# Performance work log

Hardware: AMD Instinct MI355X
Metric: run time of the kernel (lower is better)

Reference implementation:

```python
import jax, jax.numpy as jnp
import numpy as np

C = 256; G = 16; GC = C // G; K = 3; P = K * K
N = 4; H = 64; W = 64
PAD = 1; OFFSET_SCALE = 1.0; LN_EPS = 1e-5


def setup_inputs() -> dict:
    key = jax.random.key(0)
    ks = jax.random.split(key, 8)
    s = 0.02
    return {
        "x": jax.random.normal(ks[0], (N, C, H, W), jnp.float32),
        "dw_w": jax.random.normal(ks[1], (C, 1, K, K), jnp.float32) * s,
        "dw_b": jnp.zeros((C,), jnp.float32),
        "ln_g": jnp.ones((C,), jnp.float32),
        "ln_b": jnp.zeros((C,), jnp.float32),
        "off_w": jax.random.normal(ks[2], (C, G * P * 2), jnp.float32) * s,
        "off_b": jnp.zeros((G * P * 2,), jnp.float32),
        "mask_w": jax.random.normal(ks[3], (C, G * P), jnp.float32) * s,
        "mask_b": jnp.zeros((G * P,), jnp.float32),
        "inp_w": jax.random.normal(ks[4], (C, C), jnp.float32) * s,
        "inp_b": jnp.zeros((C,), jnp.float32),
        "out_w": jax.random.normal(ks[5], (C, C), jnp.float32) * s,
        "out_b": jnp.zeros((C,), jnp.float32),
    }


def _dcnv3_nchw(x, dw_w, dw_b, ln_g, ln_b, off_w, off_b, mask_w, mask_b,
                inp_w, inp_b, out_w, out_b):
    # NCHW -> NHWC (wrapper permute)
    xn = jnp.transpose(x, (0, 2, 3, 1))                      # (N,H,W,C)
    x_proj = xn @ inp_w + inp_b                              # input_proj

    # offset/mask branch: depthwise conv (NCHW) -> LayerNorm (channels-last) -> GELU
    x1 = jax.lax.conv_general_dilated(
        x, dw_w, window_strides=(1, 1), padding=((PAD, PAD), (PAD, PAD)),
        dimension_numbers=("NCHW", "OIHW", "NCHW"), feature_group_count=C)
    x1 = jnp.transpose(x1, (0, 2, 3, 1)) + dw_b
    mu = x1.mean(-1, keepdims=True)
    var = ((x1 - mu) ** 2).mean(-1, keepdims=True)
    x1 = (x1 - mu) * jax.lax.rsqrt(var + LN_EPS) * ln_g + ln_b
    x1 = jax.nn.gelu(x1, approximate=False)

    offset = (x1 @ off_w + off_b).reshape(N, H, W, G, P, 2)  # (x,y) pairs
    mask = jax.nn.softmax((x1 @ mask_w + mask_b).reshape(N, H, W, G, P), axis=-1)

    # pad sampled feature map with zeros (F.pad before sampling)
    xp = jnp.pad(x_proj, ((0, 0), (PAD, PAD), (PAD, PAD), (0, 0)))
    Hin, Win = H + 2 * PAD, W + 2 * PAD
    xg = xp.reshape(N, Hin, Win, G, GC)

    # reference points, normalized by padded size
    ref_y = (jnp.arange(H, dtype=jnp.float32) + PAD + 0.5) / Hin
    ref_x = (jnp.arange(W, dtype=jnp.float32) + PAD + 0.5) / Win
    ref = jnp.stack([jnp.broadcast_to(ref_x[None, :], (H, W)),
                     jnp.broadcast_to(ref_y[:, None], (H, W))], -1)  # (H,W,2)

    # dilation grid: x varies in the outer loop (torch meshgrid 'ij')
    d = jnp.arange(K, dtype=jnp.float32) - (K - 1) // 2     # [-1,0,1]
    gx = jnp.repeat(d, K) / Win
    gy = jnp.tile(d, K) / Hin
    grid = jnp.stack([gx, gy], -1)                           # (P,2)

    norm = jnp.array([Win, Hin], jnp.float32)
    loc = (ref[None, :, :, None, None, :] + grid * OFFSET_SCALE
           + offset * OFFSET_SCALE / norm)                   # (N,H,W,G,P,2)

    # grid_sample bilinear, align_corners=False, zero padding
    px = loc[..., 0] * Win - 0.5
    py = loc[..., 1] * Hin - 0.5
    x0 = jnp.floor(px); y0 = jnp.floor(py)
    wx = px - x0; wy = py - y0
    x0i = x0.astype(jnp.int32); y0i = y0.astype(jnp.int32)

    n_idx = jnp.arange(N)[:, None, None, None, None]
    g_idx = jnp.arange(G)[None, None, None, :, None]

    def corner(iy, ix, w):
        valid = (iy >= 0) & (iy < Hin) & (ix >= 0) & (ix < Win)
        v = xg[n_idx, jnp.clip(iy, 0, Hin - 1), jnp.clip(ix, 0, Win - 1), g_idx]
        wgt = jnp.where(valid, w, 0.0) * mask                # fold mask into weights
        return jnp.einsum("nhwgp,nhwgpc->nhwgc", wgt, v)

    out = (corner(y0i, x0i, (1 - wy) * (1 - wx))
           + corner(y0i, x0i + 1, (1 - wy) * wx)
           + corner(y0i + 1, x0i, wy * (1 - wx))
           + corner(y0i + 1, x0i + 1, wy * wx))               # (N,H,W,G,GC)

    out = out.reshape(N, H, W, C) @ out_w + out_b            # output_proj
    return jnp.transpose(out, (0, 3, 1, 2))                  # NHWC -> NCHW


def reference(x, dw_w, dw_b, ln_g, ln_b, off_w, off_b, mask_w, mask_b,
              inp_w, inp_b, out_w, out_b):
    return _dcnv3_nchw(x, dw_w, dw_b, ln_g, ln_b, off_w, off_b,
                       mask_w, mask_b, inp_w, inp_b, out_w, out_b)
```

## Files before the change

kernel.cpp:

```cpp
#include <hip/hip_runtime.h>
#include <hip/hip_bf16.h>
#include <math.h>


using bf16x8 = __attribute__((ext_vector_type(8))) short;
using f32x4  = __attribute__((ext_vector_type(4))) float;

#define GLOBAL_AS __attribute__((address_space(1)))
#define LDS_AS    __attribute__((address_space(3)))

static __device__ inline void g2lds16(const void* g, void* l) {
  __builtin_amdgcn_global_load_lds((const GLOBAL_AS int*)g, (LDS_AS int*)l, 16, 0, 0);
}
static __device__ inline unsigned short f2bf(float v) {
  __hip_bfloat16 b = __float2bfloat16(v);
  return *reinterpret_cast<unsigned short*>(&b);
}
static __device__ inline float us2f(unsigned short u) {
  union { unsigned u; float f; } c; c.u = ((unsigned)u) << 16; return c.f;
}

__global__ __launch_bounds__(256) void prep_k(
    const float* __restrict__ inp_w, const float* __restrict__ off_w,
    const float* __restrict__ off_b, const float* __restrict__ mask_w,
    const float* __restrict__ mask_b, const float* __restrict__ out_w,
    __hip_bfloat16* __restrict__ BtI, __hip_bfloat16* __restrict__ BtOM,
    __hip_bfloat16* __restrict__ BtO, float* __restrict__ bOM)
{
  int b = blockIdx.x, t = threadIdx.x;
  if (b < 256) {
    int n = b;
    BtI[n * 256 + t] = __float2bfloat16(inp_w[t * 256 + n]);
  } else if (b < 768) {
    int n = b - 256;
    float v = 0.f;
    if (n < 288) v = off_w[t * 288 + n];
    else if (n < 432) v = mask_w[t * 144 + (n - 288)];
    BtOM[n * 256 + t] = __float2bfloat16(v);
    if (b == 256) {
      for (int idx = t; idx < 512; idx += 256) {
        float bv = (idx < 288) ? off_b[idx] : ((idx < 432) ? mask_b[idx - 288] : 0.f);
        bOM[idx] = bv;
      }
    }
  } else {
    int n = b - 768;
    BtO[n * 256 + t] = __float2bfloat16(out_w[t * 256 + n]);
  }
}

__global__ __launch_bounds__(256) void xt_k(const float* __restrict__ x,
                                            __hip_bfloat16* __restrict__ xT) {
  __shared__ float tile[32][65];
  const int hw0 = blockIdx.x * 64, c0 = blockIdx.y * 32, n4 = blockIdx.z;
  const int t = threadIdx.x;
  #pragma unroll
  for (int r = 0; r < 8; ++r) {
    int idx = t + r * 256;
    int cl = idx >> 6, wl = idx & 63;
    tile[cl][wl] = x[(size_t)n4 * 1048576 + (size_t)(c0 + cl) * 4096 + hw0 + wl];
  }
  __syncthreads();
  #pragma unroll
  for (int r = 0; r < 2; ++r) {
    int idx = t + r * 256;
    int pixl = idx >> 3, cq = idx & 7;
    unsigned short b0 = f2bf(tile[cq * 4 + 0][pixl]);
    unsigned short b1 = f2bf(tile[cq * 4 + 1][pixl]);
    unsigned short b2 = f2bf(tile[cq * 4 + 2][pixl]);
    unsigned short b3 = f2bf(tile[cq * 4 + 3][pixl]);
    uint2 u;
    u.x = (unsigned)b0 | ((unsigned)b1 << 16);
    u.y = (unsigned)b2 | ((unsigned)b3 << 16);
    *(uint2*)&xT[((size_t)n4 * 4096 + hw0 + pixl) * 256 + c0 + cq * 4] = u;
  }
}

template<int CMODE>
__global__ __launch_bounds__(256) void gemm_mfma(
    const __hip_bfloat16* __restrict__ A, const __hip_bfloat16* __restrict__ Bt,
    const float* __restrict__ bias, void* __restrict__ Cv, int ldc, int nstore)
{
  __shared__ __align__(16) char smem[16512];
  short* As = (short*)smem;
  short* Bs = (short*)(smem + 8192);
  float* tb = (float*)smem;
  const int t = threadIdx.x;
  const int wave = t >> 6, lane = t & 63;
  const int quad = lane >> 4, lr = lane & 15;
  const int wm = wave >> 1, wn = wave & 1;
  const size_t m0 = (size_t)blockIdx.y * 128;
  const int n0 = blockIdx.x * 128;

  f32x4 acc[4][4];
  #pragma unroll
  for (int i = 0; i < 4; ++i)
    #pragma unroll
    for (int j = 0; j < 4; ++j)
      acc[i][j] = (f32x4){0.f, 0.f, 0.f, 0.f};

  const int srow = wave * 32;
  for (int kt = 0; kt < 256; kt += 32) {
    #pragma unroll
    for (int j = 0; j < 2; ++j) {
      int chunk = j * 64 + lane;
      int row = srow + (chunk >> 2), kq = chunk & 3;
      const __hip_bfloat16* gA = A + (m0 + row) * 256 + kt + kq * 8;
      const __hip_bfloat16* gB = Bt + (size_t)(n0 + row) * 256 + kt + kq * 8;
      g2lds16(gA, (char*)As + wave * 2048 + j * 1024);
      g2lds16(gB, (char*)Bs + wave * 2048 + j * 1024);
    }
    __syncthreads();
    bf16x8 bfv[4];
    #pragma unroll
    for (int ni = 0; ni < 4; ++ni)
      bfv[ni] = *(const bf16x8*)&Bs[(wn * 64 + ni * 16 + lr) * 32 + quad * 8];
    #pragma unroll
    for (int mi = 0; mi < 4; ++mi) {
      bf16x8 af = *(const bf16x8*)&As[(wm * 64 + mi * 16 + lr) * 32 + quad * 8];
      #pragma unroll
      for (int ni = 0; ni < 4; ++ni)
        acc[mi][ni] = __builtin_amdgcn_mfma_f32_16x16x32_bf16(af, bfv[ni], acc[mi][ni], 0, 0, 0);
    }
    __syncthreads();
  }

  if (CMODE == 2) {
    #pragma unroll
    for (int mi = 0; mi < 4; ++mi) {
      #pragma unroll
      for (int ni = 0; ni < 4; ++ni) {
        int col = n0 + wn * 64 + ni * 16 + lr;
        if (col < nstore) {
          float bv = bias[col];
          #pragma unroll
          for (int reg = 0; reg < 4; ++reg) {
            size_t m = m0 + wm * 64 + mi * 16 + quad * 4 + reg;
            ((__hip_bfloat16*)Cv)[m * ldc + col] =
                __float2bfloat16(acc[mi][ni][reg] + bv);
          }
        }
      }
    }
  } else {
    const int n4 = (int)(m0 >> 12), hw0 = (int)(m0 & 4095);
    for (int qc = 0; qc < 4; ++qc) {
      __syncthreads();
      if (wn == (qc >> 1)) {
        #pragma unroll
        for (int nis = 0; nis < 2; ++nis) {
          int ni = 2 * (qc & 1) + nis;
          int col = n0 + wn * 64 + ni * 16 + lr;
          float bv = bias[col];
          int cl = nis * 16 + lr;
          #pragma unroll
          for (int mi = 0; mi < 4; ++mi)
            #pragma unroll
            for (int reg = 0; reg < 4; ++reg) {
              int ml = wm * 64 + mi * 16 + quad * 4 + reg;
              tb[cl * 129 + ml] = acc[mi][ni][reg] + bv;
            }
        }
      }
      __syncthreads();
      #pragma unroll
      for (int r = 0; r < 4; ++r) {
        int f4i = t + r * 256;
        int row = f4i >> 5, mc = (f4i & 31) * 4;
        int co = n0 + qc * 32 + row;
        float4 v;
        v.x = tb[row * 129 + mc + 0];
        v.y = tb[row * 129 + mc + 1];
        v.z = tb[row * 129 + mc + 2];
        v.w = tb[row * 129 + mc + 3];
        *(float4*)&((float*)Cv)[(size_t)(n4 * 256 + co) * 4096 + hw0 + mc] = v;
      }
    }
  }
}

__global__ __launch_bounds__(256) void dwconv_k(
    const float* __restrict__ x, const float* __restrict__ dw_w,
    const float* __restrict__ dw_b, __hip_bfloat16* __restrict__ y)
{
  __shared__ float pl[4096];
  const int bc = blockIdx.x;
  const int n4 = bc >> 8, c = bc & 255;
  const int t = threadIdx.x;
  const float* xc = x + (size_t)n4 * 1048576 + (size_t)c * 4096;
  #pragma unroll
  for (int r = 0; r < 4; ++r) {
    int idx4 = t + r * 256;
    *(float4*)&pl[idx4 * 4] = *(const float4*)&xc[idx4 * 4];
  }
  float wv[9];
  #pragma unroll
  for (int i = 0; i < 9; ++i) wv[i] = dw_w[c * 9 + i];
  const float bb = dw_b[c];
  __syncthreads();
  __hip_bfloat16* yc = y + (size_t)(n4 * 256 + c) * 4096;
  #pragma unroll 4
  for (int r = 0; r < 16; ++r) {
    int px = t + r * 256;
    int h = px >> 6, w = px & 63;
    float s = bb;
    #pragma unroll
    for (int dh = -1; dh <= 1; ++dh) {
      int hh = h + dh;
      if ((unsigned)hh >= 64u) continue;
      #pragma unroll
      for (int dw = -1; dw <= 1; ++dw) {
        int ww = w + dw;
        if ((unsigned)ww >= 64u) continue;
        s = fmaf(pl[hh * 64 + ww], wv[(dh + 1) * 3 + (dw + 1)], s);
      }
    }
    yc[px] = __float2bfloat16(s);
  }
}

__global__ __launch_bounds__(1024) void ln_k(
    const __hip_bfloat16* __restrict__ y, const float* __restrict__ ln_g,
    const float* __restrict__ ln_b, __hip_bfloat16* __restrict__ x1)
{
  __shared__ unsigned short ys[256 * 66];
  __shared__ float gs[256], bs2[256];
  __shared__ float ps[16][64], pq[16][64], mu_s[64], rs_s[64];
  const int blk = blockIdx.x;
  const int n4 = blk >> 6, h = blk & 63;
  const int t = threadIdx.x;

  if (t < 256) { gs[t] = ln_g[t]; bs2[t] = ln_b[t]; }

  const __hip_bfloat16* yb = y + (size_t)n4 * 1048576 + h * 64;
  #pragma unroll
  for (int r = 0; r < 2; ++r) {
    int idx = t + r * 1024;
    int c = idx >> 3, w8 = idx & 7;
    uint4 u = *(const uint4*)(yb + (size_t)c * 4096 + w8 * 8);
    unsigned* d = (unsigned*)&ys[c * 66 + w8 * 8];
    d[0] = u.x; d[1] = u.y; d[2] = u.z; d[3] = u.w;
  }
  __syncthreads();

  const int w = t & 63, q = t >> 6;
  {
    float s1 = 0.f, s2 = 0.f;
    #pragma unroll
    for (int i = 0; i < 16; ++i) {
      float v = us2f(ys[(q * 16 + i) * 66 + w]);
      s1 += v; s2 = fmaf(v, v, s2);
    }
    ps[q][w] = s1; pq[q][w] = s2;
  }
  __syncthreads();
  if (t < 64) {
    float a = 0.f, b = 0.f;
    #pragma unroll
    for (int j = 0; j < 16; ++j) { a += ps[j][t]; b += pq[j][t]; }
    float mu = a * (1.f / 256.f);
    mu_s[t] = mu;
    rs_s[t] = rsqrtf(b * (1.f / 256.f) - mu * mu + 1e-5f);
  }
  __syncthreads();

  const float mu = mu_s[w], rs = rs_s[w];
  #pragma unroll
  for (int i = 0; i < 16; ++i) {
    int c = q * 16 + i;
    float v = us2f(ys[c * 66 + w]);
    float yv = fmaf((v - mu) * rs, gs[c], bs2[c]);
    float ge = 0.5f * yv * (1.f + erff(yv * 0.70710678f));
    ys[c * 66 + w] = f2bf(ge);
  }
  __syncthreads();

  const size_t row0 = ((size_t)n4 * 4096 + (size_t)h * 64) * 256;
  #pragma unroll
  for (int r = 0; r < 2; ++r) {
    int idx = t + r * 1024;
    int pix = idx >> 5, co8 = idx & 31;
    unsigned short v0 = ys[(co8 * 8 + 0) * 66 + pix];
    unsigned short v1 = ys[(co8 * 8 + 1) * 66 + pix];
    unsigned short v2 = ys[(co8 * 8 + 2) * 66 + pix];
    unsigned short v3 = ys[(co8 * 8 + 3) * 66 + pix];
    unsigned short v4 = ys[(co8 * 8 + 4) * 66 + pix];
    unsigned short v5 = ys[(co8 * 8 + 5) * 66 + pix];
    unsigned short v6 = ys[(co8 * 8 + 6) * 66 + pix];
    unsigned short v7 = ys[(co8 * 8 + 7) * 66 + pix];
    uint4 u;
    u.x = (unsigned)v0 | ((unsigned)v1 << 16);
    u.y = (unsigned)v2 | ((unsigned)v3 << 16);
    u.z = (unsigned)v4 | ((unsigned)v5 << 16);
    u.w = (unsigned)v6 | ((unsigned)v7 << 16);
    *(uint4*)&x1[row0 + (size_t)pix * 256 + co8 * 8] = u;
  }
}

__global__ __launch_bounds__(256) void sample_k(
    const __hip_bfloat16* __restrict__ xpu, const __hip_bfloat16* __restrict__ om,
    __hip_bfloat16* __restrict__ samp)
{
  __shared__ unsigned short oms[16 * 448];
  const int bid = blockIdx.x;
  const int region = bid & 7;
  const int q = bid >> 3;
  const int pix0 = region * 2048 + q * 16;
  const int t = threadIdx.x;

  {
    const uint4* gsrc = (const uint4*)(om + (size_t)pix0 * 448);
    uint4* ldst = (uint4*)oms;
    #pragma unroll
    for (int r = 0; r < 4; ++r) {
      int i = t + r * 256;
      if (i < 896) ldst[i] = gsrc[i];
    }
  }
  __syncthreads();

  const int g = t & 15;
  const int pl = t >> 4;
  const int pix = pix0 + pl;
  const int n4 = pix >> 12;
  const int hw = pix & 4095;
  const int h = hw >> 6, w = hw & 63;

  float mk[9];
  {
    const unsigned short* mp = &oms[pl * 448 + 288 + g * 9];
    float mx = -1e30f;
    #pragma unroll
    for (int p = 0; p < 9; ++p) { mk[p] = us2f(mp[p]); mx = fmaxf(mx, mk[p]); }
    float se = 0.f;
    #pragma unroll
    for (int p = 0; p < 9; ++p) { mk[p] = __expf(mk[p] - mx); se += mk[p]; }
    float inv = 1.f / se;
    #pragma unroll
    for (int p = 0; p < 9; ++p) mk[p] *= inv;
  }

  const unsigned short* op = &oms[pl * 448 + g * 18];
  const __hip_bfloat16* xpg = xpu + (g << 4);
  float ax[16];
  #pragma unroll
  for (int i = 0; i < 16; ++i) ax[i] = 0.f;

  auto corner = [&](int iy, int ix, float wt) {
    if ((unsigned)(iy - 1) >= 64u || (unsigned)(ix - 1) >= 64u) return;
    const __hip_bfloat16* src =
        xpg + ((size_t)((n4 << 12) + (iy - 1) * 64 + (ix - 1)) << 8);
    uint4 u0 = *(const uint4*)src;
    uint4 u1 = *(const uint4*)(src + 8);
    const unsigned uu[8] = {u0.x, u0.y, u0.z, u0.w, u1.x, u1.y, u1.z, u1.w};
    #pragma unroll
    for (int i = 0; i < 8; ++i) {
      float lo = us2f((unsigned short)(uu[i] & 0xffff));
      float hi = us2f((unsigned short)(uu[i] >> 16));
      ax[2 * i + 0] = fmaf(wt, lo, ax[2 * i + 0]);
      ax[2 * i + 1] = fmaf(wt, hi, ax[2 * i + 1]);
    }
  };

  #pragma unroll
  for (int p = 0; p < 9; ++p) {
    float ox = us2f(op[2 * p]), oy = us2f(op[2 * p + 1]);
    float px = (float)(w + p / 3) + ox;
    float py = (float)(h + p % 3) + oy;
    float xf = floorf(px), yf = floorf(py);
    float wx = px - xf, wy = py - yf;
    int ix = (int)xf, iy = (int)yf;
    float m = mk[p];
    corner(iy,     ix,     (1.f - wy) * (1.f - wx) * m);
    corner(iy,     ix + 1, (1.f - wy) * wx * m);
    corner(iy + 1, ix,     wy * (1.f - wx) * m);
    corner(iy + 1, ix + 1, wy * wx * m);
  }

  unsigned short ub[16];
  #pragma unroll
  for (int i = 0; i < 16; ++i) ub[i] = f2bf(ax[i]);
  uint4* d4 = (uint4*)(samp + (size_t)pix * 256 + (g << 4));
  uint4 u0, u1;
  u0.x = (unsigned)ub[0] | ((unsigned)ub[1] << 16);
  u0.y = (unsigned)ub[2] | ((unsigned)ub[3] << 16);
  u0.z = (unsigned)ub[4] | ((unsigned)ub[5] << 16);
  u0.w = (unsigned)ub[6] | ((unsigned)ub[7] << 16);
  u1.x = (unsigned)ub[8] | ((unsigned)ub[9] << 16);
  u1.y = (unsigned)ub[10] | ((unsigned)ub[11] << 16);
  u1.z = (unsigned)ub[12] | ((unsigned)ub[13] << 16);
  u1.w = (unsigned)ub[14] | ((unsigned)ub[15] << 16);
  d4[0] = u0; d4[1] = u1;
}

extern "C" void kernel_launch(void* const* d_in, const int* in_sizes, int n_in,
                              void* d_out, int out_size, void* d_ws, size_t ws_size,
                              hipStream_t stream) {
  const float* x      = (const float*)d_in[0];
  const float* dw_w   = (const float*)d_in[1];
  const float* dw_b   = (const float*)d_in[2];
  const float* ln_g   = (const float*)d_in[3];
  const float* ln_b   = (const float*)d_in[4];
  const float* off_w  = (const float*)d_in[5];
  const float* off_b  = (const float*)d_in[6];
  const float* mask_w = (const float*)d_in[7];
  const float* mask_b = (const float*)d_in[8];
  const float* inp_w  = (const float*)d_in[9];
  const float* inp_b  = (const float*)d_in[10];
  const float* out_w  = (const float*)d_in[11];
  const float* out_b  = (const float*)d_in[12];
  float* out = (float*)d_out;

  char* w0 = (char*)d_ws;
  __hip_bfloat16* xpu  = (__hip_bfloat16*)(w0);
  __hip_bfloat16* y    = (__hip_bfloat16*)(w0 + 8388608);
  __hip_bfloat16* x1   = (__hip_bfloat16*)(w0 + 16777216);
  __hip_bfloat16* xT   = (__hip_bfloat16*)(w0 + 25165824);
  __hip_bfloat16* samp = xT;
  __hip_bfloat16* om   = (__hip_bfloat16*)(w0 + 33554432);
  __hip_bfloat16* BtI  = (__hip_bfloat16*)(w0 + 48234496);
  __hip_bfloat16* BtOM = (__hip_bfloat16*)(w0 + 48365568);
  __hip_bfloat16* BtO  = (__hip_bfloat16*)(w0 + 48627712);
  float*          bOM  = (float*)(w0 + 48758784);
  if (ws_size < 48760832) return;

  prep_k<<<1024, 256, 0, stream>>>(inp_w, off_w, off_b, mask_w, mask_b, out_w,
                                   BtI, BtOM, BtO, bOM);
  xt_k<<<dim3(64, 8, 4), 256, 0, stream>>>(x, xT);
  gemm_mfma<2><<<dim3(2, 128), 256, 0, stream>>>(xT, BtI, inp_b, xpu, 256, 256);
  dwconv_k<<<1024, 256, 0, stream>>>(x, dw_w, dw_b, y);
  ln_k<<<256, 1024, 0, stream>>>(y, ln_g, ln_b, x1);
  gemm_mfma<2><<<dim3(4, 128), 256, 0, stream>>>(x1, BtOM, bOM, om, 448, 432);
  sample_k<<<1024, 256, 0, stream>>>(xpu, om, samp);
  gemm_mfma<3><<<dim3(2, 128), 256, 0, stream>>>(samp, BtO, out_b, out, 0, 256);
}
```

Before: 173.0 us.

## Shrink GEMM tiles to 64x64 and merge input/offset-mask projections into one launch

Replaces the 128x128-tile MFMA GEMM template with 64x64-tile kernels, giving four to eight times as many blocks. The input projection and the offset/mask projection now share one launch that picks its operands from blockIdx.x, which removes a launch and lets the two GEMMs run at the same time on the 256 CUs. The output projection uses the smaller tile with a resized LDS transpose epilogue. The price is less data reuse per block and more global loads of the A and B tiles per unit of MFMA work.

Result: faster. 168.7 us (-2.5%).

```diff
diff --git a/kernel.cpp b/kernel.cpp
--- a/kernel.cpp
+++ b/kernel.cpp
@@ -76,105 +76,127 @@
   }
 }
 
-template<int CMODE>
-__global__ __launch_bounds__(256) void gemm_mfma(
-    const __hip_bfloat16* __restrict__ A, const __hip_bfloat16* __restrict__ Bt,
-    const float* __restrict__ bias, void* __restrict__ Cv, int ldc, int nstore)
-{
-  __shared__ __align__(16) char smem[16512];
+struct G64 {
+  f32x4 acc[2][2];
+  int wave, lane, quad, lr, wm, wn;
+};
+
+static __device__ inline void g64_loop(
+    G64& g, const __hip_bfloat16* __restrict__ A,
+    const __hip_bfloat16* __restrict__ Bt, size_t m0, int n0,
+    short* As, short* Bs, int t)
+{
+  #pragma unroll
+  for (int i = 0; i < 2; ++i)
+    #pragma unroll
+    for (int j = 0; j < 2; ++j)
+      g.acc[i][j] = (f32x4){0.f, 0.f, 0.f, 0.f};
+  const int row = t >> 2, kq = t & 3;
+  for (int kt = 0; kt < 256; kt += 32) {
+    g2lds16(A + (m0 + row) * 256 + kt + kq * 8, (char*)As + t * 16);
+    g2lds16(Bt + (size_t)(n0 + row) * 256 + kt + kq * 8, (char*)Bs + t * 16);
+    __syncthreads();
+    bf16x8 bfv[2];
+    #pragma unroll
+    for (int ni = 0; ni < 2; ++ni)
+      bfv[ni] = *(const bf16x8*)&Bs[(g.wn * 32 + ni * 16 + g.lr) * 32 + g.quad * 8];
+    #pragma unroll
+    for (int mi = 0; mi < 2; ++mi) {
+      bf16x8 af = *(const bf16x8*)&As[(g.wm * 32 + mi * 16 + g.lr) * 32 + g.quad * 8];
+      #pragma unroll
+      for (int ni = 0; ni < 2; ++ni)
+        g.acc[mi][ni] = __builtin_amdgcn_mfma_f32_16x16x32_bf16(af, bfv[ni], g.acc[mi][ni], 0, 0, 0);
+    }
+    __syncthreads();
+  }
+}
+
+__global__ __launch_bounds__(256) void gemm_iom(
+    const __hip_bfloat16* __restrict__ xT, const __hip_bfloat16* __restrict__ x1,
+    const __hip_bfloat16* __restrict__ BtI, const __hip_bfloat16* __restrict__ BtOM,
+    const float* __restrict__ inp_b, const float* __restrict__ bOM,
+    __hip_bfloat16* __restrict__ xpu, __hip_bfloat16* __restrict__ om)
+{
+  __shared__ __align__(16) char smem[8192];
   short* As = (short*)smem;
-  short* Bs = (short*)(smem + 8192);
-  float* tb = (float*)smem;
-  const int t = threadIdx.x;
-  const int wave = t >> 6, lane = t & 63;
-  const int quad = lane >> 4, lr = lane & 15;
-  const int wm = wave >> 1, wn = wave & 1;
-  const size_t m0 = (size_t)blockIdx.y * 128;
-  const int n0 = blockIdx.x * 128;
-
-  f32x4 acc[4][4];
-  #pragma unroll
-  for (int i = 0; i < 4; ++i)
-    #pragma unroll
-    for (int j = 0; j < 4; ++j)
-      acc[i][j] = (f32x4){0.f, 0.f, 0.f, 0.f};
-
-  const int srow = wave * 32;
-  for (int kt = 0; kt < 256; kt += 32) {
-    #pragma unroll
-    for (int j = 0; j < 2; ++j) {
-      int chunk = j * 64 + lane;
-      int row = srow + (chunk >> 2), kq = chunk & 3;
-      const __hip_bfloat16* gA = A + (m0 + row) * 256 + kt + kq * 8;
-      const __hip_bfloat16* gB = Bt + (size_t)(n0 + row) * 256 + kt + kq * 8;
-      g2lds16(gA, (char*)As + wave * 2048 + j * 1024);
-      g2lds16(gB, (char*)Bs + wave * 2048 + j * 1024);
-    }
-    __syncthreads();
-    bf16x8 bfv[4];
-    #pragma unroll
-    for (int ni = 0; ni < 4; ++ni)
-      bfv[ni] = *(const bf16x8*)&Bs[(wn * 64 + ni * 16 + lr) * 32 + quad * 8];
-    #pragma unroll
-    for (int mi = 0; mi < 4; ++mi) {
-      bf16x8 af = *(const bf16x8*)&As[(wm * 64 + mi * 16 + lr) * 32 + quad * 8];
-      #pragma unroll
-      for (int ni = 0; ni < 4; ++ni)
-        acc[mi][ni] = __builtin_amdgcn_mfma_f32_16x16x32_bf16(af, bfv[ni], acc[mi][ni], 0, 0, 0);
-    }
-    __syncthreads();
-  }
-
-  if (CMODE == 2) {
-    #pragma unroll
-    for (int mi = 0; mi < 4; ++mi) {
-      #pragma unroll
-      for (int ni = 0; ni < 4; ++ni) {
-        int col = n0 + wn * 64 + ni * 16 + lr;
-        if (col < nstore) {
-          float bv = bias[col];
-          #pragma unroll
-          for (int reg = 0; reg < 4; ++reg) {
-            size_t m = m0 + wm * 64 + mi * 16 + quad * 4 + reg;
-            ((__hip_bfloat16*)Cv)[m * ldc + col] =
-                __float2bfloat16(acc[mi][ni][reg] + bv);
-          }
+  short* Bs = (short*)(smem + 4096);
+  const int t = threadIdx.x;
+  const int bx = blockIdx.x;
+  const size_t m0 = (size_t)blockIdx.y * 64;
+
+  const __hip_bfloat16* A;  const __hip_bfloat16* Bt;
+  const float* bias;        __hip_bfloat16* C;
+  int ldc, nst, n0;
+  if (bx < 4) { A = xT; Bt = BtI;  bias = inp_b; C = xpu; ldc = 256; nst = 256; n0 = bx * 64; }
+  else        { A = x1; Bt = BtOM; bias = bOM;   C = om;  ldc = 448; nst = 432; n0 = (bx - 4) * 64; }
+
+  G64 g;
+  g.wave = t >> 6; g.lane = t & 63; g.quad = g.lane >> 4; g.lr = g.lane & 15;
+  g.wm = g.wave >> 1; g.wn = g.wave & 1;
+  g64_loop(g, A, Bt, m0, n0, As, Bs, t);
+
+  #pragma unroll
+  for (int mi = 0; mi < 2; ++mi) {
+    #pragma unroll
+    for (int ni = 0; ni < 2; ++ni) {
+      int col = n0 + g.wn * 32 + ni * 16 + g.lr;
+      if (col < nst) {
+        float bv = bias[col];
+        #pragma unroll
+        for (int reg = 0; reg < 4; ++reg) {
+          size_t m = m0 + g.wm * 32 + mi * 16 + g.quad * 4 + reg;
+          C[m * ldc + col] = __float2bfloat16(g.acc[mi][ni][reg] + bv);
         }
       }
     }
-  } else {
-    const int n4 = (int)(m0 >> 12), hw0 = (int)(m0 & 4095);
-    for (int qc = 0; qc < 4; ++qc) {
-      __syncthreads();
-      if (wn == (qc >> 1)) {
+  }
+}
+
+__global__ __launch_bounds__(256) void gemm_o(
+    const __hip_bfloat16* __restrict__ samp, const __hip_bfloat16* __restrict__ BtO,
+    const float* __restrict__ out_b, float* __restrict__ out)
+{
+  __shared__ __align__(16) char smem[8448];
+  short* As = (short*)smem;
+  short* Bs = (short*)(smem + 4096);
+  float* tb = (float*)smem;
+  const int t = threadIdx.x;
+  const int n0 = blockIdx.x * 64;
+  const size_t m0 = (size_t)blockIdx.y * 64;
+
+  G64 g;
+  g.wave = t >> 6; g.lane = t & 63; g.quad = g.lane >> 4; g.lr = g.lane & 15;
+  g.wm = g.wave >> 1; g.wn = g.wave & 1;
+  g64_loop(g, samp, BtO, m0, n0, As, Bs, t);
+
+  const int n4 = (int)(m0 >> 12), hw0 = (int)(m0 & 4095);
+  for (int qc = 0; qc < 2; ++qc) {
+    __syncthreads();
+    if (g.wn == qc) {
+      #pragma unroll
+      for (int ni = 0; ni < 2; ++ni) {
+        int cl = ni * 16 + g.lr;
+        float bv = out_b[n0 + qc * 32 + cl];
         #pragma unroll
-        for (int nis = 0; nis < 2; ++nis) {
-          int ni = 2 * (qc & 1) + nis;
-          int col = n0 + wn * 64 + ni * 16 + lr;
-          float bv = bias[col];
-          int cl = nis * 16 + lr;
+        for (int mi = 0; mi < 2; ++mi)
           #pragma unroll
-          for (int mi = 0; mi < 4; ++mi)
-            #pragma unroll
-            for (int reg = 0; reg < 4; ++reg) {
-              int ml = wm * 64 + mi * 16 + quad * 4 + reg;
-              tb[cl * 129 + ml] = acc[mi][ni][reg] + bv;
-            }
-        }
+          for (int reg = 0; reg < 4; ++reg)
+            tb[cl * 65 + g.wm * 32 + mi * 16 + g.quad * 4 + reg] =
+                g.acc[mi][ni][reg] + bv;
       }
-      __syncthreads();
-      #pragma unroll
-      for (int r = 0; r < 4; ++r) {
-        int f4i = t + r * 256;
-        int row = f4i >> 5, mc = (f4i & 31) * 4;
-        int co = n0 + qc * 32 + row;
-        float4 v;
-        v.x = tb[row * 129 + mc + 0];
-        v.y = tb[row * 129 + mc + 1];
-        v.z = tb[row * 129 + mc + 2];
-        v.w = tb[row * 129 + mc + 3];
-        *(float4*)&((float*)Cv)[(size_t)(n4 * 256 + co) * 4096 + hw0 + mc] = v;
-      }
+    }
+    __syncthreads();
+    #pragma unroll
+    for (int r = 0; r < 2; ++r) {
+      int idx = t + r * 256;
+      int row = idx >> 4, mc = (idx & 15) * 4;
+      int co = n0 + qc * 32 + row;
+      float4 v;
+      v.x = tb[row * 65 + mc + 0];
+      v.y = tb[row * 65 + mc + 1];
+      v.z = tb[row * 65 + mc + 2];
+      v.w = tb[row * 65 + mc + 3];
+      *(float4*)&out[(size_t)(n4 * 256 + co) * 4096 + hw0 + mc] = v;
     }
   }
 }
@@ -427,10 +449,9 @@
   prep_k<<<1024, 256, 0, stream>>>(inp_w, off_w, off_b, mask_w, mask_b, out_w,
                                    BtI, BtOM, BtO, bOM);
   xt_k<<<dim3(64, 8, 4), 256, 0, stream>>>(x, xT);
-  gemm_mfma<2><<<dim3(2, 128), 256, 0, stream>>>(xT, BtI, inp_b, xpu, 256, 256);
   dwconv_k<<<1024, 256, 0, stream>>>(x, dw_w, dw_b, y);
   ln_k<<<256, 1024, 0, stream>>>(y, ln_g, ln_b, x1);
-  gemm_mfma<2><<<dim3(4, 128), 256, 0, stream>>>(x1, BtOM, bOM, om, 448, 432);
+  gemm_iom<<<dim3(11, 256), 256, 0, stream>>>(xT, x1, BtI, BtOM, inp_b, bOM, xpu, om);
   sample_k<<<1024, 256, 0, stream>>>(xpu, om, samp);
-  gemm_mfma<3><<<dim3(2, 128), 256, 0, stream>>>(samp, BtO, out_b, out, 0, 256);
-}
+  gemm_o<<<dim3(4, 256), 256, 0, stream>>>(samp, BtO, out_b, out);
+}
```
